# Kernel tuning notes

Measured on AMD Instinct MI355X. Metric: run time of the kernel, lower is better.

## Reference

```python
import jax, jax.numpy as jnp
import numpy as np

TEMP = 0.05
MOMENTUM = 0.2
EPS = 1e-12
B, D, N = 256, 2048, 30000


def setup_inputs() -> dict:
    key = jax.random.key(0)
    k1, k2, k3 = jax.random.split(key, 3)
    inputs = jax.random.normal(k1, (B, D), dtype=jnp.float32)
    feats = jax.random.normal(k2, (N, D), dtype=jnp.float32)
    # cluster memory bank rows are unit-normalized in practice
    feats = feats / (jnp.linalg.norm(feats, axis=1, keepdims=True) + EPS)
    targets = jax.random.randint(k3, (B,), 0, N, dtype=jnp.int64)
    return {"inputs": inputs, "features": feats, "targets": targets}


def reference(inputs, features, targets):
    # F.normalize(inputs, dim=1)
    x = inputs / (jnp.linalg.norm(inputs, axis=1, keepdims=True) + EPS)
    # outputs = x @ features.T / temp  -> [B, N]
    logits = jnp.einsum("bd,nd->bn", x, features) / TEMP
    # loss = F.cross_entropy(outputs, targets)
    logp = jax.nn.log_softmax(logits, axis=1)
    loss = -jnp.mean(jnp.take_along_axis(logp, targets[:, None], axis=1))

    # CM backward side effect: sequential per-sample momentum update + renorm of bank.
    # features[y] = m*features[y] + (1-m)*x ; features[y] /= ||features[y]||
    def step(bank, xy):
        xi, yi = xy
        f = MOMENTUM * bank[yi] + (1.0 - MOMENTUM) * xi
        f = f / (jnp.linalg.norm(f) + EPS)
        return bank.at[yi].set(f), None

    new_features, _ = jax.lax.scan(step, features, (x, targets))
    return loss, new_features
```

## Files before the change

kernel.cpp:

```cpp
#include <hip/hip_runtime.h>
#include <hip/hip_bf16.h>

#define B_ 256
#define D_ 2048
#define N_ 30000
#define INV_TEMP 20.0f
#define MOM 0.2f
#define EPSF 1e-12f
#define BN 48
#define KC 64
#define NT 625

typedef __attribute__((ext_vector_type(8))) short bf16x8;
typedef __attribute__((ext_vector_type(4))) float f32x4;

__device__ __forceinline__ unsigned short f2bf(float f) {
  union { float f; unsigned int u; } v; v.f = f;
  unsigned int u = v.u;
  unsigned int r = (u + 0x7fffu + ((u >> 16) & 1u)) >> 16;
  return (unsigned short)r;
}

__device__ __forceinline__ float blockReduceSum256(float v) {
  __shared__ float red[4];
  #pragma unroll
  for (int m = 32; m >= 1; m >>= 1) v += __shfl_xor(v, m, 64);
  int lane = threadIdx.x & 63, w = threadIdx.x >> 6;
  __syncthreads();
  if (lane == 0) red[w] = v;
  __syncthreads();
  return red[0] + red[1] + red[2] + red[3];
}

__global__ __launch_bounds__(256) void knorm(const float* __restrict__ in,
                                             float* __restrict__ x,
                                             unsigned short* __restrict__ xbf) {
  int b = blockIdx.x, t = threadIdx.x;
  const float* row = in + (size_t)b * D_;
  float vals[8]; float ss = 0.f;
  #pragma unroll
  for (int i = 0; i < 8; i++) { float f = row[t + i * 256]; vals[i] = f; ss += f * f; }
  float tot = blockReduceSum256(ss);
  float inv = 1.0f / (sqrtf(tot) + EPSF);
  #pragma unroll
  for (int i = 0; i < 8; i++) {
    float xv = vals[i] * inv;
    x[(size_t)b * D_ + t + i * 256] = xv;
    xbf[(size_t)b * D_ + t + i * 256] = f2bf(xv);
  }
}

__global__ __launch_bounds__(256) void kmain(const float* __restrict__ feats,
                                             const unsigned short* __restrict__ xbf,
                                             float* __restrict__ outF,
                                             float* __restrict__ pmax,
                                             float* __restrict__ psum) {
  __shared__ __align__(16) unsigned short xs[256 * KC];
  __shared__ __align__(16) unsigned short fs[BN * KC];
  int tid = threadIdx.x;
  int wave = tid >> 6, lane = tid & 63;
  int n0 = blockIdx.x * BN;

  f32x4 acc[4][3];
  #pragma unroll
  for (int i = 0; i < 4; i++)
    #pragma unroll
    for (int j = 0; j < 3; j++) acc[i][j] = f32x4{0.f, 0.f, 0.f, 0.f};

  for (int k0 = 0; k0 < D_; k0 += KC) {
    __syncthreads();
    #pragma unroll
    for (int i = 0; i < 8; i++) {
      int fi = tid + i * 256;
      int b = fi >> 3, g = fi & 7;
      uint4 v = *(const uint4*)(xbf + (size_t)b * D_ + k0 + g * 8);
      int byte = b * 128 + ((g * 16) ^ ((b & 7) << 4));
      *(uint4*)((char*)xs + byte) = v;
    }
    #pragma unroll
    for (int i = 0; i < 3; i++) {
      int fi = tid + i * 256;
      int n = fi >> 4, kk = (fi & 15) * 4;
      int row = n0 + n;
      const float4 v = *(const float4*)(feats + (size_t)row * D_ + k0 + kk);
      float* o = outF + (size_t)row * D_ + k0 + kk;
      o[0] = v.x; o[1] = v.y; o[2] = v.z; o[3] = v.w;
      ushort2 p0 = make_ushort2(f2bf(v.x), f2bf(v.y));
      ushort2 p1 = make_ushort2(f2bf(v.z), f2bf(v.w));
      int byte = n * 128 + ((kk * 2) ^ ((n & 7) << 4));
      *(ushort2*)((char*)fs + byte) = p0;
      *(ushort2*)((char*)fs + byte + 4) = p1;
    }
    __syncthreads();
    #pragma unroll
    for (int ks = 0; ks < 2; ks++) {
      int kbyte = (ks * 32 + ((lane >> 4) << 3)) * 2;
      bf16x8 a[4], bb[3];
      #pragma unroll
      for (int mi = 0; mi < 4; mi++) {
        int row = wave * 64 + mi * 16 + (lane & 15);
        a[mi] = *(const bf16x8*)((char*)xs + row * 128 + (kbyte ^ ((row & 7) << 4)));
      }
      #pragma unroll
      for (int ni = 0; ni < 3; ni++) {
        int row = ni * 16 + (lane & 15);
        bb[ni] = *(const bf16x8*)((char*)fs + row * 128 + (kbyte ^ ((row & 7) << 4)));
      }
      #pragma unroll
      for (int mi = 0; mi < 4; mi++)
        #pragma unroll
        for (int ni = 0; ni < 3; ni++)
          acc[mi][ni] = __builtin_amdgcn_mfma_f32_16x16x32_bf16(a[mi], bb[ni], acc[mi][ni], 0, 0, 0);
    }
  }

  int g = lane >> 4, c = lane & 15;
  #pragma unroll
  for (int mi = 0; mi < 4; mi++) {
    #pragma unroll
    for (int r = 0; r < 4; r++) {
      float v0 = acc[mi][0][r] * INV_TEMP;
      float v1 = acc[mi][1][r] * INV_TEMP;
      float v2 = acc[mi][2][r] * INV_TEMP;
      float mx = fmaxf(fmaxf(v0, v1), v2);
      #pragma unroll
      for (int m = 8; m >= 1; m >>= 1) mx = fmaxf(mx, __shfl_xor(mx, m, 64));
      float s = __expf(v0 - mx) + __expf(v1 - mx) + __expf(v2 - mx);
      #pragma unroll
      for (int m = 8; m >= 1; m >>= 1) s += __shfl_xor(s, m, 64);
      if (c == 0) {
        int row = wave * 64 + mi * 16 + g * 4 + r;
        pmax[(size_t)row * NT + blockIdx.x] = mx;
        psum[(size_t)row * NT + blockIdx.x] = s;
      }
    }
  }
}

__global__ __launch_bounds__(256) void ktdot(const float* __restrict__ feats,
                                             const float* __restrict__ x,
                                             const int* __restrict__ tgt,
                                             float* __restrict__ tdot) {
  int b = blockIdx.x, t = threadIdx.x;
  int y = tgt[b];
  const float* fr = feats + (size_t)y * D_;
  const float* xr = x + (size_t)b * D_;
  float s = 0.f;
  #pragma unroll
  for (int i = 0; i < 8; i++) s += fr[t + i * 256] * xr[t + i * 256];
  float tot = blockReduceSum256(s);
  if (t == 0) tdot[b] = tot * INV_TEMP;
}

__global__ __launch_bounds__(256) void kloss1(const float* __restrict__ pmax,
                                              const float* __restrict__ psum,
                                              const float* __restrict__ tdot,
                                              float* __restrict__ lb) {
  int b = blockIdx.x, t = threadIdx.x;
  float m = -INFINITY, s = 0.f;
  for (int i = t; i < NT; i += 256) {
    float mt = pmax[(size_t)b * NT + i];
    float st = psum[(size_t)b * NT + i];
    if (mt > m) { s = s * __expf(m - mt) + st; m = mt; }
    else        { s += st * __expf(mt - m); }
  }
  #pragma unroll
  for (int w = 32; w >= 1; w >>= 1) {
    float mo = __shfl_xor(m, w, 64);
    float so = __shfl_xor(s, w, 64);
    float M = fmaxf(m, mo);
    s = s * __expf(m - M) + so * __expf(mo - M);
    m = M;
  }
  __shared__ float sm[4], ssum[4];
  int lane = t & 63, w = t >> 6;
  if (lane == 0) { sm[w] = m; ssum[w] = s; }
  __syncthreads();
  if (t == 0) {
    float M = fmaxf(fmaxf(sm[0], sm[1]), fmaxf(sm[2], sm[3]));
    float S = ssum[0] * __expf(sm[0] - M) + ssum[1] * __expf(sm[1] - M) +
              ssum[2] * __expf(sm[2] - M) + ssum[3] * __expf(sm[3] - M);
    lb[b] = M + logf(S) - tdot[b];
  }
}

__global__ __launch_bounds__(256) void kloss2(const float* __restrict__ lb,
                                              float* __restrict__ out) {
  int t = threadIdx.x;
  float tot = blockReduceSum256(lb[t]);
  if (t == 0) out[0] = tot * (1.0f / 256.0f);
}

__global__ __launch_bounds__(256) void kupdate(const float* __restrict__ feats,
                                               const float* __restrict__ x,
                                               const int* __restrict__ tgt,
                                               float* __restrict__ outF) {
  int b = blockIdx.x, t = threadIdx.x;
  int y = tgt[b];
  for (int i = 0; i < b; i++) if (tgt[i] == y) return;
  float f[8];
  #pragma unroll
  for (int i = 0; i < 8; i++) f[i] = feats[(size_t)y * D_ + t + i * 256];
  for (int b2 = b; b2 < B_; b2++) {
    if (tgt[b2] != y) continue;
    float ss = 0.f;
    #pragma unroll
    for (int i = 0; i < 8; i++) {
      f[i] = MOM * f[i] + (1.0f - MOM) * x[(size_t)b2 * D_ + t + i * 256];
      ss += f[i] * f[i];
    }
    float tot = blockReduceSum256(ss);
    float inv = 1.0f / (sqrtf(tot) + EPSF);
    #pragma unroll
    for (int i = 0; i < 8; i++) f[i] *= inv;
  }
  #pragma unroll
  for (int i = 0; i < 8; i++) outF[(size_t)y * D_ + t + i * 256] = f[i];
}

extern "C" void kernel_launch(void* const* d_in, const int* in_sizes, int n_in,
                              void* d_out, int out_size, void* d_ws, size_t ws_size,
                              hipStream_t stream) {
  const float* inputs = (const float*)d_in[0];
  const float* feats  = (const float*)d_in[1];
  const int*   tgt    = (const int*)d_in[2];
  float* out  = (float*)d_out;
  float* outF = out + 1;

  char* ws = (char*)d_ws;
  float*          x    = (float*)ws;
  unsigned short* xbf  = (unsigned short*)(ws + (size_t)B_ * D_ * 4);
  float*          pmax = (float*)(ws + (size_t)B_ * D_ * 4 + (size_t)B_ * D_ * 2);
  float*          psum = pmax + (size_t)B_ * NT;
  float*          tdot = psum + (size_t)B_ * NT;
  float*          lb   = tdot + B_;

  hipLaunchKernelGGL(knorm,   dim3(B_),  dim3(256), 0, stream, inputs, x, xbf);
  hipLaunchKernelGGL(kmain,   dim3(NT),  dim3(256), 0, stream, feats, xbf, outF, pmax, psum);
  hipLaunchKernelGGL(ktdot,   dim3(B_),  dim3(256), 0, stream, feats, x, tgt, tdot);
  hipLaunchKernelGGL(kloss1,  dim3(B_),  dim3(256), 0, stream, pmax, psum, tdot, lb);
  hipLaunchKernelGGL(kloss2,  dim3(1),   dim3(256), 0, stream, lb, out);
  hipLaunchKernelGGL(kupdate, dim3(B_),  dim3(256), 0, stream, feats, x, tgt, outF);
}
```

Baseline: 204.2 us.

## Double-buffer GEMM tiles with direct global-to-LDS loads and 512-thread blocks

Restructures the main logits kernel to double-buffer the x and feature tiles in shared memory. The next k-chunk is prefetched while MFMAs run on the current one, so each iteration needs one barrier instead of two. The x tile is now loaded with global_load_lds, which writes straight into LDS and skips the register round trip. Blocks grow to 512 threads, each wave owning 32 rows, and the feature copy to the output is reshaped into float2 stores shifted by one element, with a lane shuffle to handle the odd alignment. This doubles shared memory per block, which may reduce occupancy, and the shifted-store indexing adds complexity.

After: 240.3 us. 17.7% more time.

```diff
diff --git a/kernel.cpp b/kernel.cpp
--- a/kernel.cpp
+++ b/kernel.cpp
@@ -10,9 +10,14 @@
 #define BN 48
 #define KC 64
 #define NT 625
+#define NK 32
 
 typedef __attribute__((ext_vector_type(8))) short bf16x8;
 typedef __attribute__((ext_vector_type(4))) float f32x4;
+
+typedef const __attribute__((address_space(1))) void* gas_t;
+typedef __attribute__((address_space(3))) void* las_t;
+#define GLOAD16(g, l) __builtin_amdgcn_global_load_lds((gas_t)(g), (las_t)(l), 16, 0, 0)
 
 __device__ __forceinline__ unsigned short f2bf(float f) {
   union { float f; unsigned int u; } v; v.f = f;
@@ -50,73 +55,102 @@
   }
 }
 
-__global__ __launch_bounds__(256) void kmain(const float* __restrict__ feats,
-                                             const unsigned short* __restrict__ xbf,
-                                             float* __restrict__ outF,
-                                             float* __restrict__ pmax,
-                                             float* __restrict__ psum) {
-  __shared__ __align__(16) unsigned short xs[256 * KC];
-  __shared__ __align__(16) unsigned short fs[BN * KC];
-  int tid = threadIdx.x;
-  int wave = tid >> 6, lane = tid & 63;
+__global__ __launch_bounds__(512, 4) void kmain(const float* __restrict__ feats,
+                                                const unsigned short* __restrict__ xbf,
+                                                float* __restrict__ outF,
+                                                float* __restrict__ pmax,
+                                                float* __restrict__ psum) {
+  __shared__ __align__(16) unsigned short xs[2][16384];
+  __shared__ __align__(16) unsigned short fs[2][3072];
+  int tid = threadIdx.x, wave = tid >> 6, lane = tid & 63;
   int n0 = blockIdx.x * BN;
 
-  f32x4 acc[4][3];
-  #pragma unroll
-  for (int i = 0; i < 4; i++)
+  int gswz = (lane & 7) ^ (lane >> 3);
+  int bbase = wave * 8 + (lane >> 3);
+  const char* xsrc = (const char*)xbf;
+
+  f32x4 acc[2][3];
+  #pragma unroll
+  for (int i = 0; i < 2; i++)
     #pragma unroll
     for (int j = 0; j < 3; j++) acc[i][j] = f32x4{0.f, 0.f, 0.f, 0.f};
 
-  for (int k0 = 0; k0 < D_; k0 += KC) {
+  int fn[3], fc[3];
+  #pragma unroll
+  for (int i = 0; i < 3; i++) { int fi = tid + i * 512; fn[i] = fi >> 5; fc[i] = fi & 31; }
+  int sl = (lane & 32) | ((lane + 1) & 31);
+  float2 fv[3];
+
+  {
+    #pragma unroll
+    for (int i = 0; i < 3; i++)
+      fv[i] = *(const float2*)(feats + (size_t)(n0 + fn[i]) * D_ + 2 * fc[i]);
+    size_t gb = ((size_t)bbase * D_ + gswz * 8) * 2;
+    #pragma unroll
+    for (int i = 0; i < 4; i++)
+      GLOAD16(xsrc + gb + (size_t)i * 64 * D_ * 2,
+              (char*)&xs[0][0] + i * 8192 + wave * 1024);
+    #pragma unroll
+    for (int i = 0; i < 3; i++) {
+      float nx = __shfl(fv[i].x, sl, 64);
+      size_t e = (size_t)(n0 + fn[i]) * D_ + 2 * fc[i];
+      if (fc[i] < 31) *(float2*)(outF + e + 1) = make_float2(fv[i].y, nx);
+      else { outF[e + 1] = fv[i].y; outF[e - 62] = nx; }
+      ushort2 p = make_ushort2(f2bf(fv[i].x), f2bf(fv[i].y));
+      int byte = fn[i] * 128 + ((4 * fc[i]) ^ ((fn[i] & 7) << 4));
+      *(ushort2*)((char*)&fs[0][0] + byte) = p;
+    }
+  }
+  __syncthreads();
+
+  int q = lane >> 4, lr = lane & 15;
+  for (int t = 0; t < NK; t++) {
+    int cur = t & 1, nxt = cur ^ 1;
+    if (t < NK - 1) {
+      int k0 = (t + 1) * KC;
+      #pragma unroll
+      for (int i = 0; i < 3; i++)
+        fv[i] = *(const float2*)(feats + (size_t)(n0 + fn[i]) * D_ + k0 + 2 * fc[i]);
+      size_t gb = ((size_t)bbase * D_ + k0 + gswz * 8) * 2;
+      #pragma unroll
+      for (int i = 0; i < 4; i++)
+        GLOAD16(xsrc + gb + (size_t)i * 64 * D_ * 2,
+                (char*)&xs[nxt][0] + i * 8192 + wave * 1024);
+    }
+    #pragma unroll
+    for (int ks = 0; ks < 2; ks++) {
+      int g = ks * 4 + q;
+      bf16x8 a0, a1, b0, b1, b2;
+      { int row = wave * 32 + lr;      a0 = *(const bf16x8*)((char*)&xs[cur][0] + row * 128 + ((g * 16) ^ ((row & 7) << 4))); }
+      { int row = wave * 32 + 16 + lr; a1 = *(const bf16x8*)((char*)&xs[cur][0] + row * 128 + ((g * 16) ^ ((row & 7) << 4))); }
+      { int row = lr;                  b0 = *(const bf16x8*)((char*)&fs[cur][0] + row * 128 + ((g * 16) ^ ((row & 7) << 4))); }
+      { int row = 16 + lr;             b1 = *(const bf16x8*)((char*)&fs[cur][0] + row * 128 + ((g * 16) ^ ((row & 7) << 4))); }
+      { int row = 32 + lr;             b2 = *(const bf16x8*)((char*)&fs[cur][0] + row * 128 + ((g * 16) ^ ((row & 7) << 4))); }
+      acc[0][0] = __builtin_amdgcn_mfma_f32_16x16x32_bf16(a0, b0, acc[0][0], 0, 0, 0);
+      acc[0][1] = __builtin_amdgcn_mfma_f32_16x16x32_bf16(a0, b1, acc[0][1], 0, 0, 0);
+      acc[0][2] = __builtin_amdgcn_mfma_f32_16x16x32_bf16(a0, b2, acc[0][2], 0, 0, 0);
+      acc[1][0] = __builtin_amdgcn_mfma_f32_16x16x32_bf16(a1, b0, acc[1][0], 0, 0, 0);
+      acc[1][1] = __builtin_amdgcn_mfma_f32_16x16x32_bf16(a1, b1, acc[1][1], 0, 0, 0);
+      acc[1][2] = __builtin_amdgcn_mfma_f32_16x16x32_bf16(a1, b2, acc[1][2], 0, 0, 0);
+    }
+    if (t < NK - 1) {
+      int k0 = (t + 1) * KC;
+      #pragma unroll
+      for (int i = 0; i < 3; i++) {
+        float nx = __shfl(fv[i].x, sl, 64);
+        size_t e = (size_t)(n0 + fn[i]) * D_ + k0 + 2 * fc[i];
+        if (fc[i] < 31) *(float2*)(outF + e + 1) = make_float2(fv[i].y, nx);
+        else { outF[e + 1] = fv[i].y; outF[e - 62] = nx; }
+        ushort2 p = make_ushort2(f2bf(fv[i].x), f2bf(fv[i].y));
+        int byte = fn[i] * 128 + ((4 * fc[i]) ^ ((fn[i] & 7) << 4));
+        *(ushort2*)((char*)&fs[nxt][0] + byte) = p;
+      }
+    }
     __syncthreads();
-    #pragma unroll
-    for (int i = 0; i < 8; i++) {
-      int fi = tid + i * 256;
-      int b = fi >> 3, g = fi & 7;
-      uint4 v = *(const uint4*)(xbf + (size_t)b * D_ + k0 + g * 8);
-      int byte = b * 128 + ((g * 16) ^ ((b & 7) << 4));
-      *(uint4*)((char*)xs + byte) = v;
-    }
-    #pragma unroll
-    for (int i = 0; i < 3; i++) {
-      int fi = tid + i * 256;
-      int n = fi >> 4, kk = (fi & 15) * 4;
-      int row = n0 + n;
-      const float4 v = *(const float4*)(feats + (size_t)row * D_ + k0 + kk);
-      float* o = outF + (size_t)row * D_ + k0 + kk;
-      o[0] = v.x; o[1] = v.y; o[2] = v.z; o[3] = v.w;
-      ushort2 p0 = make_ushort2(f2bf(v.x), f2bf(v.y));
-      ushort2 p1 = make_ushort2(f2bf(v.z), f2bf(v.w));
-      int byte = n * 128 + ((kk * 2) ^ ((n & 7) << 4));
-      *(ushort2*)((char*)fs + byte) = p0;
-      *(ushort2*)((char*)fs + byte + 4) = p1;
-    }
-    __syncthreads();
-    #pragma unroll
-    for (int ks = 0; ks < 2; ks++) {
-      int kbyte = (ks * 32 + ((lane >> 4) << 3)) * 2;
-      bf16x8 a[4], bb[3];
-      #pragma unroll
-      for (int mi = 0; mi < 4; mi++) {
-        int row = wave * 64 + mi * 16 + (lane & 15);
-        a[mi] = *(const bf16x8*)((char*)xs + row * 128 + (kbyte ^ ((row & 7) << 4)));
-      }
-      #pragma unroll
-      for (int ni = 0; ni < 3; ni++) {
-        int row = ni * 16 + (lane & 15);
-        bb[ni] = *(const bf16x8*)((char*)fs + row * 128 + (kbyte ^ ((row & 7) << 4)));
-      }
-      #pragma unroll
-      for (int mi = 0; mi < 4; mi++)
-        #pragma unroll
-        for (int ni = 0; ni < 3; ni++)
-          acc[mi][ni] = __builtin_amdgcn_mfma_f32_16x16x32_bf16(a[mi], bb[ni], acc[mi][ni], 0, 0, 0);
-    }
-  }
-
-  int g = lane >> 4, c = lane & 15;
-  #pragma unroll
-  for (int mi = 0; mi < 4; mi++) {
+  }
+
+  #pragma unroll
+  for (int mi = 0; mi < 2; mi++) {
     #pragma unroll
     for (int r = 0; r < 4; r++) {
       float v0 = acc[mi][0][r] * INV_TEMP;
@@ -128,8 +162,8 @@
       float s = __expf(v0 - mx) + __expf(v1 - mx) + __expf(v2 - mx);
       #pragma unroll
       for (int m = 8; m >= 1; m >>= 1) s += __shfl_xor(s, m, 64);
-      if (c == 0) {
-        int row = wave * 64 + mi * 16 + g * 4 + r;
+      if (lr == 0) {
+        int row = wave * 32 + mi * 16 + q * 4 + r;
         pmax[(size_t)row * NT + blockIdx.x] = mx;
         psum[(size_t)row * NT + blockIdx.x] = s;
       }
@@ -236,7 +270,7 @@
   float*          lb   = tdot + B_;
 
   hipLaunchKernelGGL(knorm,   dim3(B_),  dim3(256), 0, stream, inputs, x, xbf);
-  hipLaunchKernelGGL(kmain,   dim3(NT),  dim3(256), 0, stream, feats, xbf, outF, pmax, psum);
+  hipLaunchKernelGGL(kmain,   dim3(NT),  dim3(512), 0, stream, feats, xbf, outF, pmax, psum);
   hipLaunchKernelGGL(ktdot,   dim3(B_),  dim3(256), 0, stream, feats, x, tgt, tdot);
   hipLaunchKernelGGL(kloss1,  dim3(B_),  dim3(256), 0, stream, pmax, psum, tdot, lb);
   hipLaunchKernelGGL(kloss2,  dim3(1),   dim3(256), 0, stream, lb, out);
```

## Drop LDS staging in main GEMM; load operands straight into MFMA registers

Applied to the files above, without the earlier changes.

Rewrites the main logits kernel to use 384 threads (6 waves, a 2x3 split of batch halves by feature sub-tiles). Each wave loads its feature rows directly from global memory into registers, prefetching the next K chunk, and reads the bf16 x operand straight from global/L2 instead of staging both through shared memory with two barriers per K step. The fp32 copy of the bank into the output is done by one wave group with lane shuffles that realign the output by one float, since the output starts at out+1, and then uses vector stores. Per-wave softmax partials are merged across the three waves in LDS before being written. This removes LDS traffic and synchronisation, at the cost of redundant global reads of x and more register pressure.

After: 439.7 us. 115% more time.

```diff
diff --git a/kernel.cpp b/kernel.cpp
--- a/kernel.cpp
+++ b/kernel.cpp
@@ -10,6 +10,7 @@
 #define BN 48
 #define KC 64
 #define NT 625
+#define NK 32
 
 typedef __attribute__((ext_vector_type(8))) short bf16x8;
 typedef __attribute__((ext_vector_type(4))) float f32x4;
@@ -21,6 +22,15 @@
   return (unsigned short)r;
 }
 
+__device__ __forceinline__ bf16x8 pack8(float4 a, float4 b) {
+  bf16x8 r;
+  r[0] = (short)f2bf(a.x); r[1] = (short)f2bf(a.y);
+  r[2] = (short)f2bf(a.z); r[3] = (short)f2bf(a.w);
+  r[4] = (short)f2bf(b.x); r[5] = (short)f2bf(b.y);
+  r[6] = (short)f2bf(b.z); r[7] = (short)f2bf(b.w);
+  return r;
+}
+
 __device__ __forceinline__ float blockReduceSum256(float v) {
   __shared__ float red[4];
   #pragma unroll
@@ -50,90 +60,97 @@
   }
 }
 
-__global__ __launch_bounds__(256) void kmain(const float* __restrict__ feats,
-                                             const unsigned short* __restrict__ xbf,
-                                             float* __restrict__ outF,
-                                             float* __restrict__ pmax,
-                                             float* __restrict__ psum) {
-  __shared__ __align__(16) unsigned short xs[256 * KC];
-  __shared__ __align__(16) unsigned short fs[BN * KC];
-  int tid = threadIdx.x;
-  int wave = tid >> 6, lane = tid & 63;
+__global__ __launch_bounds__(384, 3) void kmain(const float* __restrict__ feats,
+                                                const unsigned short* __restrict__ xbf,
+                                                float* __restrict__ outp,
+                                                float* __restrict__ pmax,
+                                                float* __restrict__ psum) {
+  __shared__ float pm[3][256], ps[3][256];
+  int tid = threadIdx.x, wave = tid >> 6, lane = tid & 63;
+  int mh = wave / 3, nw = wave % 3;
+  int q = lane >> 4, lr = lane & 15;
   int n0 = blockIdx.x * BN;
-
-  f32x4 acc[4][3];
-  #pragma unroll
-  for (int i = 0; i < 4; i++)
-    #pragma unroll
-    for (int j = 0; j < 3; j++) acc[i][j] = f32x4{0.f, 0.f, 0.f, 0.f};
-
-  for (int k0 = 0; k0 < D_; k0 += KC) {
-    __syncthreads();
-    #pragma unroll
-    for (int i = 0; i < 8; i++) {
-      int fi = tid + i * 256;
-      int b = fi >> 3, g = fi & 7;
-      uint4 v = *(const uint4*)(xbf + (size_t)b * D_ + k0 + g * 8);
-      int byte = b * 128 + ((g * 16) ^ ((b & 7) << 4));
-      *(uint4*)((char*)xs + byte) = v;
-    }
-    #pragma unroll
-    for (int i = 0; i < 3; i++) {
-      int fi = tid + i * 256;
-      int n = fi >> 4, kk = (fi & 15) * 4;
-      int row = n0 + n;
-      const float4 v = *(const float4*)(feats + (size_t)row * D_ + k0 + kk);
-      float* o = outF + (size_t)row * D_ + k0 + kk;
-      o[0] = v.x; o[1] = v.y; o[2] = v.z; o[3] = v.w;
-      ushort2 p0 = make_ushort2(f2bf(v.x), f2bf(v.y));
-      ushort2 p1 = make_ushort2(f2bf(v.z), f2bf(v.w));
-      int byte = n * 128 + ((kk * 2) ^ ((n & 7) << 4));
-      *(ushort2*)((char*)fs + byte) = p0;
-      *(ushort2*)((char*)fs + byte + 4) = p1;
-    }
-    __syncthreads();
+  int nrow = n0 + nw * 16 + lr;
+  const float* fbase = feats + (size_t)nrow * D_;
+  int sl = (lane + 16) & 63;
+
+  f32x4 acc[8];
+  #pragma unroll
+  for (int i = 0; i < 8; i++) acc[i] = f32x4{0.f, 0.f, 0.f, 0.f};
+
+  float4 fv[2][2];
+  #pragma unroll
+  for (int ks = 0; ks < 2; ks++) {
+    fv[ks][0] = *(const float4*)(fbase + ks * 32 + q * 8);
+    fv[ks][1] = *(const float4*)(fbase + ks * 32 + q * 8 + 4);
+  }
+
+  for (int t = 0; t < NK; t++) {
+    bf16x8 bcur[2];
+    #pragma unroll
+    for (int ks = 0; ks < 2; ks++) bcur[ks] = pack8(fv[ks][0], fv[ks][1]);
+
+    if (mh == 0) {
+      #pragma unroll
+      for (int ks = 0; ks < 2; ks++) {
+        int K = t * KC + ks * 32;
+        float4 A = fv[ks][0], Bv = fv[ks][1];
+        float nx = __shfl(A.x, sl, 64);
+        float ny = __shfl(A.y, sl, 64);
+        float nz = __shfl(A.z, sl, 64);
+        size_t rb = (size_t)nrow * D_ + K;
+        *(float4*)(outp + rb + 4 * (2 * q + 1)) = make_float4(A.w, Bv.x, Bv.y, Bv.z);
+        if (q < 3) *(float4*)(outp + rb + 4 * (2 * q + 2)) = make_float4(Bv.w, nx, ny, nz);
+        if (q == 0) { outp[rb + 1] = A.x; outp[rb + 2] = A.y; outp[rb + 3] = A.z; }
+        if (q == 3) outp[rb + 32] = Bv.w;
+      }
+    }
+
+    int tn = (t + 1 < NK) ? t + 1 : t;
     #pragma unroll
     for (int ks = 0; ks < 2; ks++) {
-      int kbyte = (ks * 32 + ((lane >> 4) << 3)) * 2;
-      bf16x8 a[4], bb[3];
-      #pragma unroll
-      for (int mi = 0; mi < 4; mi++) {
-        int row = wave * 64 + mi * 16 + (lane & 15);
-        a[mi] = *(const bf16x8*)((char*)xs + row * 128 + (kbyte ^ ((row & 7) << 4)));
+      fv[ks][0] = *(const float4*)(fbase + tn * KC + ks * 32 + q * 8);
+      fv[ks][1] = *(const float4*)(fbase + tn * KC + ks * 32 + q * 8 + 4);
+    }
+
+    #pragma unroll
+    for (int ks = 0; ks < 2; ks++) {
+      bf16x8 a[8];
+      size_t ab = (size_t)(mh * 128 + lr) * D_ + t * KC + ks * 32 + q * 8;
+      #pragma unroll
+      for (int mi = 0; mi < 8; mi++)
+        a[mi] = *(const bf16x8*)(xbf + ab + (size_t)mi * 16 * D_);
+      #pragma unroll
+      for (int mi = 0; mi < 8; mi++)
+        acc[mi] = __builtin_amdgcn_mfma_f32_16x16x32_bf16(a[mi], bcur[ks], acc[mi], 0, 0, 0);
+    }
+  }
+
+  #pragma unroll
+  for (int mi = 0; mi < 8; mi++) {
+    #pragma unroll
+    for (int r = 0; r < 4; r++) {
+      float v = acc[mi][r] * INV_TEMP;
+      float mx = v;
+      #pragma unroll
+      for (int m = 8; m >= 1; m >>= 1) mx = fmaxf(mx, __shfl_xor(mx, m, 64));
+      float s = __expf(v - mx);
+      #pragma unroll
+      for (int m = 8; m >= 1; m >>= 1) s += __shfl_xor(s, m, 64);
+      if (lr == 0) {
+        int row = mh * 128 + mi * 16 + q * 4 + r;
+        pm[nw][row] = mx; ps[nw][row] = s;
       }
-      #pragma unroll
-      for (int ni = 0; ni < 3; ni++) {
-        int row = ni * 16 + (lane & 15);
-        bb[ni] = *(const bf16x8*)((char*)fs + row * 128 + (kbyte ^ ((row & 7) << 4)));
-      }
-      #pragma unroll
-      for (int mi = 0; mi < 4; mi++)
-        #pragma unroll
-        for (int ni = 0; ni < 3; ni++)
-          acc[mi][ni] = __builtin_amdgcn_mfma_f32_16x16x32_bf16(a[mi], bb[ni], acc[mi][ni], 0, 0, 0);
-    }
-  }
-
-  int g = lane >> 4, c = lane & 15;
-  #pragma unroll
-  for (int mi = 0; mi < 4; mi++) {
-    #pragma unroll
-    for (int r = 0; r < 4; r++) {
-      float v0 = acc[mi][0][r] * INV_TEMP;
-      float v1 = acc[mi][1][r] * INV_TEMP;
-      float v2 = acc[mi][2][r] * INV_TEMP;
-      float mx = fmaxf(fmaxf(v0, v1), v2);
-      #pragma unroll
-      for (int m = 8; m >= 1; m >>= 1) mx = fmaxf(mx, __shfl_xor(mx, m, 64));
-      float s = __expf(v0 - mx) + __expf(v1 - mx) + __expf(v2 - mx);
-      #pragma unroll
-      for (int m = 8; m >= 1; m >>= 1) s += __shfl_xor(s, m, 64);
-      if (c == 0) {
-        int row = wave * 64 + mi * 16 + g * 4 + r;
-        pmax[(size_t)row * NT + blockIdx.x] = mx;
-        psum[(size_t)row * NT + blockIdx.x] = s;
-      }
-    }
+    }
+  }
+  __syncthreads();
+  if (tid < 256) {
+    float m0 = pm[0][tid], m1 = pm[1][tid], m2 = pm[2][tid];
+    float M = fmaxf(fmaxf(m0, m1), m2);
+    float S = ps[0][tid] * __expf(m0 - M) + ps[1][tid] * __expf(m1 - M) +
+              ps[2][tid] * __expf(m2 - M);
+    pmax[(size_t)tid * NT + blockIdx.x] = M;
+    psum[(size_t)tid * NT + blockIdx.x] = S;
   }
 }
 
@@ -236,7 +253,7 @@
   float*          lb   = tdot + B_;
 
   hipLaunchKernelGGL(knorm,   dim3(B_),  dim3(256), 0, stream, inputs, x, xbf);
-  hipLaunchKernelGGL(kmain,   dim3(NT),  dim3(256), 0, stream, feats, xbf, outF, pmax, psum);
+  hipLaunchKernelGGL(kmain,   dim3(NT),  dim3(384), 0, stream, feats, xbf, out, pmax, psum);
   hipLaunchKernelGGL(ktdot,   dim3(B_),  dim3(256), 0, stream, feats, x, tgt, tdot);
   hipLaunchKernelGGL(kloss1,  dim3(B_),  dim3(256), 0, stream, pmax, psum, tdot, lb);
   hipLaunchKernelGGL(kloss2,  dim3(1),   dim3(256), 0, stream, lb, out);
```

## Shrink N-tile to 16, load x via global_load_lds, vectorize aligned bank copy

Applied to the files above, without the earlier changes.

The main GEMM kernel drops its feature tile from 48 to 16 rows, which triples the grid and adds an occupancy hint in launch bounds. The bf16 x tile now goes straight from global memory into LDS through global_load_lds with swizzled addressing. The copy of the feature bank into the output, which sits at a 1-float offset, now goes through lane shuffles so it can be written as aligned float4 stores instead of scalar ones. The cost is three times more re-reads of the x tile per feature row, and three times more partial max/sum entries for the loss kernels to reduce.

After: 272.7 us. 33.5% more time.

```diff
diff --git a/kernel.cpp b/kernel.cpp
--- a/kernel.cpp
+++ b/kernel.cpp
@@ -7,12 +7,17 @@
 #define INV_TEMP 20.0f
 #define MOM 0.2f
 #define EPSF 1e-12f
-#define BN 48
+#define BN 16
 #define KC 64
-#define NT 625
+#define NT 1875
+#define NK 32
 
 typedef __attribute__((ext_vector_type(8))) short bf16x8;
 typedef __attribute__((ext_vector_type(4))) float f32x4;
+
+typedef const __attribute__((address_space(1))) void* gas_t;
+typedef __attribute__((address_space(3))) void* las_t;
+#define GLOAD16(g, l) __builtin_amdgcn_global_load_lds((gas_t)(g), (las_t)(l), 16, 0, 0)
 
 __device__ __forceinline__ unsigned short f2bf(float f) {
   union { float f; unsigned int u; } v; v.f = f;
@@ -50,86 +55,86 @@
   }
 }
 
-__global__ __launch_bounds__(256) void kmain(const float* __restrict__ feats,
-                                             const unsigned short* __restrict__ xbf,
-                                             float* __restrict__ outF,
-                                             float* __restrict__ pmax,
-                                             float* __restrict__ psum) {
-  __shared__ __align__(16) unsigned short xs[256 * KC];
-  __shared__ __align__(16) unsigned short fs[BN * KC];
-  int tid = threadIdx.x;
-  int wave = tid >> 6, lane = tid & 63;
+__global__ __launch_bounds__(256, 4) void kmain(const float* __restrict__ feats,
+                                                const unsigned short* __restrict__ xbf,
+                                                float* __restrict__ outp,
+                                                float* __restrict__ pmax,
+                                                float* __restrict__ psum) {
+  __shared__ __align__(16) unsigned short xs[16384];
+  __shared__ __align__(16) unsigned short fs[1024];
+  int tid = threadIdx.x, wave = tid >> 6, lane = tid & 63;
   int n0 = blockIdx.x * BN;
-
-  f32x4 acc[4][3];
-  #pragma unroll
-  for (int i = 0; i < 4; i++)
-    #pragma unroll
-    for (int j = 0; j < 3; j++) acc[i][j] = f32x4{0.f, 0.f, 0.f, 0.f};
-
-  for (int k0 = 0; k0 < D_; k0 += KC) {
+  int q = lane >> 4, lr = lane & 15;
+
+  int gswz = (lane & 7) ^ (lane >> 3);
+  int rof = wave * 8 + (lane >> 3);
+  const char* xsrc = (const char*)xbf;
+
+  int fn = tid >> 4, fcc = tid & 15;
+  const float* fbase = feats + (size_t)(n0 + fn) * D_ + 4 * fcc;
+  int sl = (lane & 48) | ((lane + 1) & 15);
+
+  f32x4 acc[4];
+  #pragma unroll
+  for (int i = 0; i < 4; i++) acc[i] = f32x4{0.f, 0.f, 0.f, 0.f};
+
+  for (int t = 0; t < NK; t++) {
+    int k0 = t * KC;
     __syncthreads();
-    #pragma unroll
-    for (int i = 0; i < 8; i++) {
-      int fi = tid + i * 256;
-      int b = fi >> 3, g = fi & 7;
-      uint4 v = *(const uint4*)(xbf + (size_t)b * D_ + k0 + g * 8);
-      int byte = b * 128 + ((g * 16) ^ ((b & 7) << 4));
-      *(uint4*)((char*)xs + byte) = v;
-    }
-    #pragma unroll
-    for (int i = 0; i < 3; i++) {
-      int fi = tid + i * 256;
-      int n = fi >> 4, kk = (fi & 15) * 4;
-      int row = n0 + n;
-      const float4 v = *(const float4*)(feats + (size_t)row * D_ + k0 + kk);
-      float* o = outF + (size_t)row * D_ + k0 + kk;
-      o[0] = v.x; o[1] = v.y; o[2] = v.z; o[3] = v.w;
-      ushort2 p0 = make_ushort2(f2bf(v.x), f2bf(v.y));
-      ushort2 p1 = make_ushort2(f2bf(v.z), f2bf(v.w));
-      int byte = n * 128 + ((kk * 2) ^ ((n & 7) << 4));
+    float4 fv = *(const float4*)(fbase + k0);
+    size_t gb = ((size_t)rof * D_ + k0 + gswz * 8) * 2;
+    #pragma unroll
+    for (int i = 0; i < 8; i++)
+      GLOAD16(xsrc + gb + (size_t)i * 32 * D_ * 2,
+              (char*)xs + i * 4096 + wave * 1024);
+    {
+      ushort2 p0 = make_ushort2(f2bf(fv.x), f2bf(fv.y));
+      ushort2 p1 = make_ushort2(f2bf(fv.z), f2bf(fv.w));
+      int byte = fn * 128 + ((8 * fcc) ^ ((fn & 7) << 4));
       *(ushort2*)((char*)fs + byte) = p0;
       *(ushort2*)((char*)fs + byte + 4) = p1;
     }
     __syncthreads();
     #pragma unroll
     for (int ks = 0; ks < 2; ks++) {
-      int kbyte = (ks * 32 + ((lane >> 4) << 3)) * 2;
-      bf16x8 a[4], bb[3];
+      int g = ks * 4 + q;
+      bf16x8 a[4], bb;
+      { int row = lr; bb = *(const bf16x8*)((char*)fs + row * 128 + ((g * 16) ^ ((row & 7) << 4))); }
       #pragma unroll
       for (int mi = 0; mi < 4; mi++) {
-        int row = wave * 64 + mi * 16 + (lane & 15);
-        a[mi] = *(const bf16x8*)((char*)xs + row * 128 + (kbyte ^ ((row & 7) << 4)));
+        int row = wave * 64 + mi * 16 + lr;
+        a[mi] = *(const bf16x8*)((char*)xs + row * 128 + ((g * 16) ^ ((row & 7) << 4)));
       }
       #pragma unroll
-      for (int ni = 0; ni < 3; ni++) {
-        int row = ni * 16 + (lane & 15);
-        bb[ni] = *(const bf16x8*)((char*)fs + row * 128 + (kbyte ^ ((row & 7) << 4)));
-      }
-      #pragma unroll
       for (int mi = 0; mi < 4; mi++)
-        #pragma unroll
-        for (int ni = 0; ni < 3; ni++)
-          acc[mi][ni] = __builtin_amdgcn_mfma_f32_16x16x32_bf16(a[mi], bb[ni], acc[mi][ni], 0, 0, 0);
-    }
-  }
-
-  int g = lane >> 4, c = lane & 15;
+        acc[mi] = __builtin_amdgcn_mfma_f32_16x16x32_bf16(a[mi], bb, acc[mi], 0, 0, 0);
+    }
+    {
+      float nx = __shfl(fv.x, sl, 64);
+      float ny = __shfl(fv.y, sl, 64);
+      float nz = __shfl(fv.z, sl, 64);
+      size_t rb = (size_t)(n0 + fn) * D_ + k0;
+      if (fcc < 15)
+        *(float4*)(outp + rb + 4 * fcc + 4) = make_float4(fv.w, nx, ny, nz);
+      else
+        outp[rb + 64] = fv.w;
+      if (fcc == 0) { outp[rb + 1] = fv.x; outp[rb + 2] = fv.y; outp[rb + 3] = fv.z; }
+    }
+  }
+
   #pragma unroll
   for (int mi = 0; mi < 4; mi++) {
     #pragma unroll
     for (int r = 0; r < 4; r++) {
-      float v0 = acc[mi][0][r] * INV_TEMP;
-      float v1 = acc[mi][1][r] * INV_TEMP;
-      float v2 = acc[mi][2][r] * INV_TEMP;
-      float mx = fmaxf(fmaxf(v0, v1), v2);
+      float v = acc[mi][r] * INV_TEMP;
+      float mx = v;
       #pragma unroll
       for (int m = 8; m >= 1; m >>= 1) mx = fmaxf(mx, __shfl_xor(mx, m, 64));
-      float s = __expf(v0 - mx) + __expf(v1 - mx) + __expf(v2 - mx);
+      float s = __expf(v - mx);
       #pragma unroll
       for (int m = 8; m >= 1; m >>= 1) s += __shfl_xor(s, m, 64);
-      if (c == 0) {
-        int row = wave * 64 + mi * 16 + g * 4 + r;
+      if (lr == 0) {
+        int row = wave * 64 + mi * 16 + q * 4 + r;
         pmax[(size_t)row * NT + blockIdx.x] = mx;
         psum[(size_t)row * NT + blockIdx.x] = s;
       }
@@ -236,7 +241,7 @@
   float*          lb   = tdot + B_;
 
   hipLaunchKernelGGL(knorm,   dim3(B_),  dim3(256), 0, stream, inputs, x, xbf);
-  hipLaunchKernelGGL(kmain,   dim3(NT),  dim3(256), 0, stream, feats, xbf, outF, pmax, psum);
+  hipLaunchKernelGGL(kmain,   dim3(NT),  dim3(256), 0, stream, feats, xbf, out, pmax, psum);
   hipLaunchKernelGGL(ktdot,   dim3(B_),  dim3(256), 0, stream, feats, x, tgt, tdot);
   hipLaunchKernelGGL(kloss1,  dim3(B_),  dim3(256), 0, stream, pmax, psum, tdot, lb);
   hipLaunchKernelGGL(kloss2,  dim3(1),   dim3(256), 0, stream, lb, out);
```
